# Kernel tuning notes

Hardware: AMD Instinct MI355X
Metric: run time of the kernel (lower is better)

The kernel has to match this reference:

```python
import jax, jax.numpy as jnp
import numpy as np

B, C, H, W = 8, 64, 112, 112
O, K, PAD, STRIDE = 64, 3, 1, 1
KK = K * K
OH = (H - K + 2 * PAD) // STRIDE + 1
OW = (W - K + 2 * PAD) // STRIDE + 1
L = OH * OW  # number of patches


def setup_inputs() -> dict:
    key = jax.random.key(0)
    k1, k2, k3 = jax.random.split(key, 3)
    x = jax.random.normal(k1, (B, C, H, W), dtype=jnp.float32)
    weight = jax.random.normal(k2, (O, C, K, K), dtype=jnp.float32)
    # one uniformly random kernel position to zero out, per patch (nums=1)
    mask_idx = jax.random.randint(k3, (L,), 0, KK, dtype=jnp.int32)
    return {"x": x, "weight": weight, "mask_idx": mask_idx}


def reference(x, weight, mask_idx):
    b = x.shape[0]
    # im2col: [b, C*KK, OH, OW], feature dim ordered channel-major (c, kh, kw)
    # which matches torch.nn.Unfold ordering.
    patches = jax.lax.conv_general_dilated_patches(
        x, (K, K), (STRIDE, STRIDE), ((PAD, PAD), (PAD, PAD)))
    patches = patches.reshape(b, C * KK, L)  # [b, CK, L]

    # Per-patch mask over kernel positions, tiled across channels
    # (equivalent to mask.repeat(1, in_channels) in the original).
    mask = jnp.ones((L, KK), dtype=x.dtype).at[jnp.arange(L), mask_idx].set(0.0)
    mask_full = jnp.tile(mask, (1, C))  # [L, C*KK]

    # weight.view(O, -1).t() -> [CK, O]; masking the weight rows per patch is
    # mathematically identical to masking the unfolded input per patch, which
    # avoids materializing the [L, CK, O] masked weight tensor.
    w2 = weight.reshape(O, C * KK).T  # [CK, O]
    out = jnp.einsum('bkl,lk,ko->bol', patches, mask_full, w2)  # [b, O, L]
    return out.reshape(b, O, OH, OW)
```

## Files before the change

### kernel.cpp

```cpp
#include <hip/hip_runtime.h>
#include <hip/hip_bf16.h>
#include <cstdint>

#define Bn 8
#define Cn 64
#define Hn 112
#define Wn 112
#define On 64
#define Ln (Hn * Wn)
#define HP 114
#define WP 114

typedef __attribute__((ext_vector_type(4)))  float f32x4;
typedef __attribute__((ext_vector_type(16))) float f32x16;
typedef __attribute__((ext_vector_type(8)))  short bf16x8;
typedef __attribute__((ext_vector_type(4)))  unsigned int u32x4;

typedef __attribute__((address_space(3))) unsigned int lds_u32;
typedef __attribute__((address_space(1))) const unsigned int glob_u32;

__device__ __forceinline__ unsigned f2bf(float f) {
    unsigned u = __float_as_uint(f);
    unsigned r = 0x7fffu + ((u >> 16) & 1u);
    return (u + r) >> 16;
}

__global__ __launch_bounds__(128) void prep_kernel(const float* __restrict__ x,
                                                   const float* __restrict__ w,
                                                   unsigned short* __restrict__ xps,
                                                   unsigned short* __restrict__ wpk) {
    int blk = blockIdx.x;
    int t = threadIdx.x;
    if (blk < 912) {
        int b = blk / HP, row = blk - b * HP;
        int c8  = t >> 4;
        int wpl = t & 15;
        int h = row - 1;
        const float* xb = x + (size_t)b * Cn * Hn * Wn;
        unsigned short* dst = xps + ((size_t)(b * HP + row) * WP) * Cn;
#pragma unroll
        for (int g = 0; g < 8; ++g) {
            int wp = wpl + (g << 4);
            if (wp < WP) {
                int wcol = wp - 1;
                bool inb = ((unsigned)h < (unsigned)Hn) & ((unsigned)wcol < (unsigned)Wn);
                const float* s = xb + ((size_t)(c8 * 8) * Hn + (inb ? h : 0)) * Wn + (inb ? wcol : 0);
                unsigned pk[4];
#pragma unroll
                for (int j = 0; j < 4; ++j) {
                    float v0 = s[(size_t)(2 * j)     * (Hn * Wn)];
                    float v1 = s[(size_t)(2 * j + 1) * (Hn * Wn)];
                    if (!inb) { v0 = 0.f; v1 = 0.f; }
                    pk[j] = f2bf(v0) | (f2bf(v1) << 16);
                }
                int slot = c8 ^ (wp & 7);
                u32x4 v; v[0] = pk[0]; v[1] = pk[1]; v[2] = pk[2]; v[3] = pk[3];
                *reinterpret_cast<u32x4*>(dst + ((size_t)wp * 8 + slot) * 8) = v;
            }
        }
    } else {
        int idx = (blk - 912) * 2 + (t >> 6);
        int lane = t & 63;
        int kc = idx & 3, wr2 = (idx >> 2) & 1, p = idx >> 3;
        int o  = wr2 * 32 + (lane & 31);
        int cb = kc * 16 + (lane >> 5) * 8;
        unsigned pk[4];
#pragma unroll
        for (int j = 0; j < 4; ++j) {
            float v0 = w[((size_t)o * Cn + cb + 2 * j) * 9 + p];
            float v1 = w[((size_t)o * Cn + cb + 2 * j + 1) * 9 + p];
            pk[j] = f2bf(v0) | (f2bf(v1) << 16);
        }
        u32x4 v; v[0] = pk[0]; v[1] = pk[1]; v[2] = pk[2]; v[3] = pk[3];
        reinterpret_cast<u32x4*>(wpk)[idx * 64 + lane] = v;
    }
}

__global__ __launch_bounds__(512, 4) void conv_mfma(const unsigned short* __restrict__ xps,
                                                    const unsigned short* __restrict__ wpk,
                                                    const int* __restrict__ mask_idx,
                                                    float* __restrict__ out) {
    __shared__ char xs[4 * WP * Cn * 2];

    int b  = blockIdx.x & 7;
    int lt = blockIdx.x >> 3;
    int l0 = lt * 128;
    int oh0 = l0 / Wn;

    int tid  = threadIdx.x;
    int wave = tid >> 6, lane = tid & 63;
    int wr = wave >> 2;
    int wc = wave & 3;
    int hi = lane >> 5;

    int lg = l0 + wc * 32 + (lane & 31);
    int oh = lg / Wn, ow = lg - oh * Wn;
    int r  = oh - oh0;
    int mv = mask_idx[lg];

    {
        const char* gsrc = (const char*)(xps + ((size_t)(b * HP + oh0) * WP) * Cn);
        int cb0 = wave * 456;
#pragma unroll
        for (int i = 0; i < 8; ++i) {
            int cbase = cb0 + i * 64;
            if (i < 7 || lane < 8) {
                __builtin_amdgcn_global_load_lds(
                    (glob_u32*)(gsrc + ((size_t)(cbase + lane) << 4)),
                    reinterpret_cast<lds_u32*>(reinterpret_cast<uintptr_t>(xs + ((size_t)cbase << 4))),
                    16, 0, 0);
            }
        }
    }

    const u32x4* wv = reinterpret_cast<const u32x4*>(wpk);
    u32x4 apre[2][4];
#pragma unroll
    for (int kc = 0; kc < 4; ++kc) apre[0][kc] = wv[(wr * 4 + kc) * 64 + lane];
#pragma unroll
    for (int kc = 0; kc < 4; ++kc) apre[1][kc] = wv[((2 + wr) * 4 + kc) * 64 + lane];

    f32x16 acc = {};
    const u32x4 vzero = {0u, 0u, 0u, 0u};

    __syncthreads();

#pragma unroll
    for (int p = 0; p < 9; ++p) {
        int dh = p / 3, dw = p - dh * 3;

        int wq   = ow + dw;
        int base = ((r + dh) * WP + wq) << 7;
        int swz  = (wq & 7) << 4;
        u32x4 bv[4];
#pragma unroll
        for (int kc = 0; kc < 4; ++kc) {
            int off = (base + ((2 * kc + hi) << 4)) ^ swz;
            bv[kc] = *reinterpret_cast<const u32x4*>(xs + off);
        }
        if (mv == p) { bv[0] = vzero; bv[1] = vzero; bv[2] = vzero; bv[3] = vzero; }

#pragma unroll
        for (int kc = 0; kc < 4; ++kc) {
            bf16x8 a  = *reinterpret_cast<bf16x8*>(&apre[p & 1][kc]);
            bf16x8 bb = *reinterpret_cast<bf16x8*>(&bv[kc]);
            acc = __builtin_amdgcn_mfma_f32_32x32x16_bf16(a, bb, acc, 0, 0, 0);
        }

        if (p < 7) {
#pragma unroll
            for (int kc = 0; kc < 4; ++kc)
                apre[p & 1][kc] = wv[(((p + 2) * 2 + wr) * 4 + kc) * 64 + lane];
        }
    }

    float* ob = out + (size_t)(b * On + wr * 32) * Ln + lg;
#pragma unroll
    for (int reg = 0; reg < 16; ++reg) {
        int orow = (reg & 3) + 8 * (reg >> 2) + 4 * hi;
        ob[(size_t)orow * Ln] = acc[reg];
    }
}

extern "C" void kernel_launch(void* const* d_in, const int* in_sizes, int n_in,
                              void* d_out, int out_size, void* d_ws, size_t ws_size,
                              hipStream_t stream) {
    const float* x    = (const float*)d_in[0];
    const float* w    = (const float*)d_in[1];
    const int*   mask = (const int*)d_in[2];
    float* out = (float*)d_out;

    unsigned short* xps = (unsigned short*)d_ws;
    unsigned short* wpk = (unsigned short*)((char*)d_ws + 13307904);

    prep_kernel<<<948,     128, 0, stream>>>(x, w, xps, wpk);
    conv_mfma  <<<Bn * 98, 512, 0, stream>>>(xps, wpk, mask, out);
}
```

Baseline: 97.73 us.

## Retile conv to one output row per block with 16x16x32 MFMA

The conv kernel now gives each block one output row (112 pixels) over 7 waves. Each wave computes all 64 output channels with 16x16x32 bf16 MFMAs instead of the 32x32x16 tiling over 128-pixel tiles, and only 3 padded input rows are staged in LDS instead of 4. Prep is also restructured: each thread handles one padded pixel and all 64 channels, and the weights are repacked to match the new MFMA fragment layout. This trades more weight loads per wave (each wave reloads all weights for every tap) for less LDS per block, more blocks and higher occupancy.

```diff
diff --git a/kernel.cpp b/kernel.cpp
--- a/kernel.cpp
+++ b/kernel.cpp
@@ -12,7 +12,6 @@
 #define WP 114
 
 typedef __attribute__((ext_vector_type(4)))  float f32x4;
-typedef __attribute__((ext_vector_type(16))) float f32x16;
 typedef __attribute__((ext_vector_type(8)))  short bf16x8;
 typedef __attribute__((ext_vector_type(4)))  unsigned int u32x4;
 
@@ -32,38 +31,35 @@
     int blk = blockIdx.x;
     int t = threadIdx.x;
     if (blk < 912) {
-        int b = blk / HP, row = blk - b * HP;
-        int c8  = t >> 4;
-        int wpl = t & 15;
-        int h = row - 1;
-        const float* xb = x + (size_t)b * Cn * Hn * Wn;
-        unsigned short* dst = xps + ((size_t)(b * HP + row) * WP) * Cn;
+        int b = blk / HP, hp = blk - b * HP;
+        int wp = t;
+        if (wp >= WP) return;
+        int h = hp - 1, wc = wp - 1;
+        bool inb = ((unsigned)h < (unsigned)Hn) & ((unsigned)wc < (unsigned)Wn);
+        const float* src = x + (size_t)b * Cn * Hn * Wn + (inb ? (h * Wn + wc) : 0);
+        unsigned buf[32];
 #pragma unroll
-        for (int g = 0; g < 8; ++g) {
-            int wp = wpl + (g << 4);
-            if (wp < WP) {
-                int wcol = wp - 1;
-                bool inb = ((unsigned)h < (unsigned)Hn) & ((unsigned)wcol < (unsigned)Wn);
-                const float* s = xb + ((size_t)(c8 * 8) * Hn + (inb ? h : 0)) * Wn + (inb ? wcol : 0);
-                unsigned pk[4];
+        for (int c = 0; c < Cn; c += 2) {
+            float v0 = src[(size_t)c * (Hn * Wn)];
+            float v1 = src[(size_t)(c + 1) * (Hn * Wn)];
+            if (!inb) { v0 = 0.f; v1 = 0.f; }
+            buf[c >> 1] = f2bf(v0) | (f2bf(v1) << 16);
+        }
+        unsigned short* dst = xps + ((size_t)(b * HP + hp) * WP + wp) * Cn;
+        int sw = wp & 7;
 #pragma unroll
-                for (int j = 0; j < 4; ++j) {
-                    float v0 = s[(size_t)(2 * j)     * (Hn * Wn)];
-                    float v1 = s[(size_t)(2 * j + 1) * (Hn * Wn)];
-                    if (!inb) { v0 = 0.f; v1 = 0.f; }
-                    pk[j] = f2bf(v0) | (f2bf(v1) << 16);
-                }
-                int slot = c8 ^ (wp & 7);
-                u32x4 v; v[0] = pk[0]; v[1] = pk[1]; v[2] = pk[2]; v[3] = pk[3];
-                *reinterpret_cast<u32x4*>(dst + ((size_t)wp * 8 + slot) * 8) = v;
-            }
+        for (int i = 0; i < 8; ++i) {
+            u32x4 v;
+            v[0] = buf[i * 4 + 0]; v[1] = buf[i * 4 + 1];
+            v[2] = buf[i * 4 + 2]; v[3] = buf[i * 4 + 3];
+            *reinterpret_cast<u32x4*>(dst + (size_t)(i ^ sw) * 8) = v;
         }
     } else {
         int idx = (blk - 912) * 2 + (t >> 6);
         int lane = t & 63;
-        int kc = idx & 3, wr2 = (idx >> 2) & 1, p = idx >> 3;
-        int o  = wr2 * 32 + (lane & 31);
-        int cb = kc * 16 + (lane >> 5) * 8;
+        int ki = idx & 1, of = (idx >> 1) & 3, p = idx >> 3;
+        int o  = of * 16 + (lane & 15);
+        int cb = ki * 32 + (lane >> 4) * 8;
         unsigned pk[4];
 #pragma unroll
         for (int j = 0; j < 4; ++j) {
@@ -76,89 +72,78 @@
     }
 }
 
-__global__ __launch_bounds__(512, 4) void conv_mfma(const unsigned short* __restrict__ xps,
-                                                    const unsigned short* __restrict__ wpk,
-                                                    const int* __restrict__ mask_idx,
-                                                    float* __restrict__ out) {
-    __shared__ char xs[4 * WP * Cn * 2];
+__global__ __launch_bounds__(448, 5) void conv16(const unsigned short* __restrict__ xps,
+                                                 const unsigned short* __restrict__ wpk,
+                                                 const int* __restrict__ mask_idx,
+                                                 float* __restrict__ out) {
+    __shared__ char xs[3 * WP * Cn * 2];
 
-    int b  = blockIdx.x & 7;
-    int lt = blockIdx.x >> 3;
-    int l0 = lt * 128;
-    int oh0 = l0 / Wn;
+    int b   = blockIdx.x & 7;
+    int row = blockIdx.x >> 3;
+    int tid = threadIdx.x;
+    int wave = tid >> 6, lane = tid & 63;
+    int n = lane & 15, g = lane >> 4;
 
-    int tid  = threadIdx.x;
-    int wave = tid >> 6, lane = tid & 63;
-    int wr = wave >> 2;
-    int wc = wave & 3;
-    int hi = lane >> 5;
-
-    int lg = l0 + wc * 32 + (lane & 31);
-    int oh = lg / Wn, ow = lg - oh * Wn;
-    int r  = oh - oh0;
-    int mv = mask_idx[lg];
+    int cw = wave * 16 + n;
+    int mv = mask_idx[row * Wn + cw];
 
     {
-        const char* gsrc = (const char*)(xps + ((size_t)(b * HP + oh0) * WP) * Cn);
-        int cb0 = wave * 456;
+        const char* gsrc = (const char*)(xps + ((size_t)(b * HP + row) * WP) * Cn);
 #pragma unroll
-        for (int i = 0; i < 8; ++i) {
-            int cbase = cb0 + i * 64;
-            if (i < 7 || lane < 8) {
+        for (int i = 0; i < 7; ++i) {
+            int q = tid + i * 448;
+            if (q < 3 * 8 * WP) {
                 __builtin_amdgcn_global_load_lds(
-                    (glob_u32*)(gsrc + ((size_t)(cbase + lane) << 4)),
-                    reinterpret_cast<lds_u32*>(reinterpret_cast<uintptr_t>(xs + ((size_t)cbase << 4))),
+                    (glob_u32*)(gsrc + ((size_t)q << 4)),
+                    reinterpret_cast<lds_u32*>(reinterpret_cast<uintptr_t>(
+                        xs + ((size_t)(q - lane) << 4))),
                     16, 0, 0);
             }
         }
     }
 
     const u32x4* wv = reinterpret_cast<const u32x4*>(wpk);
-    u32x4 apre[2][4];
-#pragma unroll
-    for (int kc = 0; kc < 4; ++kc) apre[0][kc] = wv[(wr * 4 + kc) * 64 + lane];
-#pragma unroll
-    for (int kc = 0; kc < 4; ++kc) apre[1][kc] = wv[((2 + wr) * 4 + kc) * 64 + lane];
-
-    f32x16 acc = {};
     const u32x4 vzero = {0u, 0u, 0u, 0u};
+    f32x4 acc[4] = {};
 
     __syncthreads();
 
 #pragma unroll
     for (int p = 0; p < 9; ++p) {
+        u32x4 av[8];
+#pragma unroll
+        for (int f = 0; f < 8; ++f) av[f] = wv[(p * 8 + f) * 64 + lane];
+
         int dh = p / 3, dw = p - dh * 3;
-
-        int wq   = ow + dw;
-        int base = ((r + dh) * WP + wq) << 7;
-        int swz  = (wq & 7) << 4;
-        u32x4 bv[4];
+        int wq = cw + dw;
+        int sw = wq & 7;
+        u32x4 bv[2];
 #pragma unroll
-        for (int kc = 0; kc < 4; ++kc) {
-            int off = (base + ((2 * kc + hi) << 4)) ^ swz;
-            bv[kc] = *reinterpret_cast<const u32x4*>(xs + off);
+        for (int kc = 0; kc < 2; ++kc) {
+            int chunk = (dh * WP + wq) * 8 + ((kc * 4 + g) ^ sw);
+            bv[kc] = *reinterpret_cast<const u32x4*>(xs + ((size_t)chunk << 4));
         }
-        if (mv == p) { bv[0] = vzero; bv[1] = vzero; bv[2] = vzero; bv[3] = vzero; }
+        if (mv == p) { bv[0] = vzero; bv[1] = vzero; }
 
 #pragma unroll
-        for (int kc = 0; kc < 4; ++kc) {
-            bf16x8 a  = *reinterpret_cast<bf16x8*>(&apre[p & 1][kc]);
-            bf16x8 bb = *reinterpret_cast<bf16x8*>(&bv[kc]);
-            acc = __builtin_amdgcn_mfma_f32_32x32x16_bf16(a, bb, acc, 0, 0, 0);
-        }
-
-        if (p < 7) {
+        for (int of = 0; of < 4; ++of) {
 #pragma unroll
-            for (int kc = 0; kc < 4; ++kc)
-                apre[p & 1][kc] = wv[(((p + 2) * 2 + wr) * 4 + kc) * 64 + lane];
+            for (int kc = 0; kc < 2; ++kc) {
+                acc[of] = __builtin_amdgcn_mfma_f32_16x16x32_bf16(
+                    *reinterpret_cast<bf16x8*>(&av[of * 2 + kc]),
+                    *reinterpret_cast<bf16x8*>(&bv[kc]), acc[of], 0, 0, 0);
+            }
         }
     }
 
-    float* ob = out + (size_t)(b * On + wr * 32) * Ln + lg;
+    float* ob = out + (size_t)(b * On) * Ln + row * Wn + cw;
 #pragma unroll
-    for (int reg = 0; reg < 16; ++reg) {
-        int orow = (reg & 3) + 8 * (reg >> 2) + 4 * hi;
-        ob[(size_t)orow * Ln] = acc[reg];
+    for (int of = 0; of < 4; ++of) {
+#pragma unroll
+        for (int reg = 0; reg < 4; ++reg) {
+            int o = of * 16 + g * 4 + reg;
+            ob[(size_t)o * Ln] = acc[of][reg];
+        }
     }
 }
 
@@ -173,6 +158,6 @@
     unsigned short* xps = (unsigned short*)d_ws;
     unsigned short* wpk = (unsigned short*)((char*)d_ws + 13307904);
 
-    prep_kernel<<<948,     128, 0, stream>>>(x, w, xps, wpk);
-    conv_mfma  <<<Bn * 98, 512, 0, stream>>>(xps, wpk, mask, out);
+    prep_kernel<<<948,      128, 0, stream>>>(x, w, xps, wpk);
+    conv16     <<<Bn * Hn,  448, 0, stream>>>(xps, wpk, mask, out);
 }
```

After: 106.2 us. 8.7% more time.
